# Kernel optimization log

Measured on AMD Instinct MI355X. Metric: run time of the kernel, lower is better.

The kernel has to match this reference:

```python
import jax, jax.numpy as jnp
import numpy as np

VOCAB = 65535
EMB = 1024
CTX = 1024
B = 32
HID = 4 * EMB


def setup_inputs() -> dict:
    key = jax.random.key(0)
    ks = jax.random.split(key, 20)
    s = 0.02
    inp = {
        "idx": jax.random.randint(ks[0], (B, 1), 0, VOCAB),
        "key_cache": jax.random.normal(ks[1], (B, CTX - 1, EMB), jnp.float32),
        "value_cache": jax.random.normal(ks[2], (B, CTX - 1, EMB), jnp.float32),
        "emb_table": jax.random.normal(ks[3], (VOCAB, EMB), jnp.float32) * s,
        "pos_table": jax.random.normal(ks[4], (CTX, EMB), jnp.float32) * s,
        "Wk": jax.random.normal(ks[5], (EMB, EMB), jnp.float32) * s,
        "bk": jnp.zeros((EMB,), jnp.float32),
        "Wv": jax.random.normal(ks[6], (EMB, EMB), jnp.float32) * s,
        "bv": jnp.zeros((EMB,), jnp.float32),
        "Wq": jax.random.normal(ks[7], (EMB, EMB), jnp.float32) * s,
        "bq": jnp.zeros((EMB,), jnp.float32),
        "W1": jax.random.normal(ks[8], (EMB, HID), jnp.float32) * s,
        "b1": jnp.zeros((HID,), jnp.float32),
        "W2": jax.random.normal(ks[9], (HID, EMB), jnp.float32) * s,
        "b2": jnp.zeros((EMB,), jnp.float32),
        "Wl": jax.random.normal(ks[10], (EMB, VOCAB), jnp.float32) * s,
        "bl": jnp.zeros((VOCAB,), jnp.float32),
    }
    return inp


def reference(idx, key_cache, value_cache, emb_table, pos_table,
              Wk, bk, Wv, bv, Wq, bq, W1, b1, W2, b2, Wl, bl):
    # token + position embeddings (seq_len=1, positions = arange(1) = [0])
    tok = emb_table[idx]                      # [B, 1, D]
    pos = pos_table[:1][None, :, :]           # [1, 1, D]
    x = tok + pos                             # [B, 1, D]

    # cache truncation to last context_size-1 steps (no-op here at 1023)
    kc = key_cache[:, -(CTX - 1):, :]
    vc = value_cache[:, -(CTX - 1):, :]

    # single-head attention with KV cache
    k_new = x @ Wk + bk                       # [B, 1, D]
    v_new = x @ Wv + bv
    q_new = x @ Wq + bq
    keys = jnp.concatenate([kc, k_new], axis=1)    # [B, S, D]
    values = jnp.concatenate([vc, v_new], axis=1)  # [B, S, D]
    scale = 1.0 / jnp.sqrt(jnp.asarray(EMB, x.dtype))
    scores = jnp.einsum("bqd,bsd->bqs", q_new, keys) * scale  # [B, 1, S]
    probs = jax.nn.softmax(scores, axis=-1)
    attn_out = jnp.einsum("bqs,bsd->bqd", probs, values)      # [B, 1, D]

    # feed-forward (exact GELU, matching torch nn.GELU default)
    h = jax.nn.gelu(attn_out @ W1 + b1, approximate=False)
    ffn_out = h @ W2 + b2                     # [B, 1, D]

    logits = ffn_out @ Wl + bl                # [B, 1, VOCAB]
    return logits
```

## Files before the change

### kernel.cpp

```cpp
#include <hip/hip_runtime.h>
#include <cstddef>

#define BATCH 32
#define EMBD 1024
#define SCTX 1023
#define CTXF 1024
#define HIDD 4096
#define VOC 65535

__global__ void embed_kernel(const int* __restrict__ idx, const float* __restrict__ emb,
                             const float* __restrict__ pos, float* __restrict__ x) {
  int b = blockIdx.x, t = threadIdx.x;
  const float4* er = (const float4*)(emb + (size_t)idx[b] * EMBD);
  const float4* pr = (const float4*)pos;
  float4 e = er[t], p = pr[t];
  ((float4*)(x + (size_t)b * EMBD))[t] = make_float4(e.x + p.x, e.y + p.y, e.z + p.z, e.w + p.w);
}

template <int CHK>
__global__ __launch_bounds__(256) void skgemm_lds(const float* __restrict__ X,
                                                  const float* __restrict__ W,
                                                  float* __restrict__ Pout, int N, int K) {
  __shared__ float xt[CHK][BATCH];
  int t = threadIdx.x;
  int p = blockIdx.y;
  int i0 = p * CHK;
  for (int m = t; m < CHK * BATCH; m += 256) {
    int i = m >> 5, b = m & 31;
    xt[i][b] = X[b * K + i0 + i];
  }
  __syncthreads();

  int j = blockIdx.x * 256 + t;
  float acc[BATCH];
#pragma unroll
  for (int b = 0; b < BATCH; ++b) acc[b] = 0.f;
  const float* wp = W + (size_t)i0 * N + j;
#pragma unroll 8
  for (int i = 0; i < CHK; ++i) {
    float w = wp[(size_t)i * N];
#pragma unroll
    for (int b = 0; b < BATCH; ++b) acc[b] = fmaf(xt[i][b], w, acc[b]);
  }
#pragma unroll
  for (int b = 0; b < BATCH; ++b) Pout[((size_t)p * BATCH + b) * N + j] = acc[b];
}

template <int CHK>
__global__ __launch_bounds__(256) void qkv_lds(const float* __restrict__ X,
                                               const float* __restrict__ Wk,
                                               const float* __restrict__ Wv,
                                               const float* __restrict__ Wq,
                                               float* __restrict__ Pout, int nch) {
  __shared__ float xt[CHK][BATCH];
  int t = threadIdx.x;
  int p = blockIdx.y;
  int i0 = p * CHK;
  for (int m = t; m < CHK * BATCH; m += 256) {
    int i = m >> 5, b = m & 31;
    xt[i][b] = X[b * EMBD + i0 + i];
  }
  __syncthreads();

  const float* __restrict__ W = (blockIdx.z == 0) ? Wk : (blockIdx.z == 1) ? Wv : Wq;
  int j = blockIdx.x * 256 + t;
  float acc[BATCH];
#pragma unroll
  for (int b = 0; b < BATCH; ++b) acc[b] = 0.f;
  const float* wp = W + (size_t)i0 * EMBD + j;
#pragma unroll 8
  for (int i = 0; i < CHK; ++i) {
    float w = wp[(size_t)i * EMBD];
#pragma unroll
    for (int b = 0; b < BATCH; ++b) acc[b] = fmaf(xt[i][b], w, acc[b]);
  }
#pragma unroll
  for (int b = 0; b < BATCH; ++b)
    Pout[((size_t)(blockIdx.z * nch + p) * BATCH + b) * EMBD + j] = acc[b];
}

__global__ void reduce_qkv(const float* __restrict__ part, int P,
                           const float* __restrict__ bk, const float* __restrict__ bv,
                           const float* __restrict__ bq,
                           float* __restrict__ kout, float* __restrict__ vout,
                           float* __restrict__ qout) {
  int z = blockIdx.y;
  int m = blockIdx.x * 256 + threadIdx.x;
  float s = 0.f;
  for (int p = 0; p < P; ++p) s += part[(size_t)(z * P + p) * (BATCH * EMBD) + m];
  const float* bias = (z == 0) ? bk : (z == 1) ? bv : bq;
  float* out = (z == 0) ? kout : (z == 1) ? vout : qout;
  out[m] = s + bias[m & (EMBD - 1)];
}

__global__ void reduce_ep(const float* __restrict__ part, int P,
                          const float* __restrict__ bias, float* __restrict__ out,
                          int total, int mask, int act) {
  int m = blockIdx.x * 256 + threadIdx.x;
  if (m >= total) return;
  float s = 0.f;
  for (int p = 0; p < P; ++p) s += part[(size_t)p * total + m];
  if (bias) s += bias[m & mask];
  if (act == 1) s = 0.5f * s * (1.f + erff(s * 0.70710678118654752f));
  out[m] = s;
}

__global__ void scores_kernel(const float* __restrict__ q, const float* __restrict__ kcache,
                              const float* __restrict__ knew, float* __restrict__ scores) {
  int b = blockIdx.y;
  int wave = threadIdx.x >> 6, lane = threadIdx.x & 63;
  const float* qb = q + (size_t)b * EMBD;
  float4 qf[4];
#pragma unroll
  for (int r = 0; r < 4; ++r) qf[r] = *(const float4*)(qb + r * 256 + lane * 4);
  int sbase = blockIdx.x * 16 + wave * 4;
  const float* kr[4];
  float acc[4] = {0.f, 0.f, 0.f, 0.f};
#pragma unroll
  for (int it = 0; it < 4; ++it) {
    int s = sbase + it;
    kr[it] = (s < SCTX) ? (kcache + ((size_t)b * SCTX + s) * EMBD)
                        : (knew + (size_t)b * EMBD);
  }
#pragma unroll
  for (int r = 0; r < 4; ++r) {
#pragma unroll
    for (int it = 0; it < 4; ++it) {
      float4 kf = *(const float4*)(kr[it] + r * 256 + lane * 4);
      acc[it] += qf[r].x * kf.x + qf[r].y * kf.y + qf[r].z * kf.z + qf[r].w * kf.w;
    }
  }
#pragma unroll
  for (int it = 0; it < 4; ++it) {
    float a = acc[it];
#pragma unroll
    for (int m = 32; m > 0; m >>= 1) a += __shfl_xor(a, m, 64);
    if (lane == 0) scores[(size_t)b * CTXF + sbase + it] = a * 0.03125f;
  }
}

__global__ void softmax_kernel(float* __restrict__ sc) {
  int b = blockIdx.x;
  int t = threadIdx.x;
  __shared__ float red[16];
  float v = sc[(size_t)b * CTXF + t];
  float m = v;
#pragma unroll
  for (int d = 32; d > 0; d >>= 1) m = fmaxf(m, __shfl_xor(m, d, 64));
  if ((t & 63) == 0) red[t >> 6] = m;
  __syncthreads();
  float bm = red[0];
#pragma unroll
  for (int w = 1; w < 16; ++w) bm = fmaxf(bm, red[w]);
  float e = expf(v - bm);
  __syncthreads();
  float s = e;
#pragma unroll
  for (int d = 32; d > 0; d >>= 1) s += __shfl_xor(s, d, 64);
  if ((t & 63) == 0) red[t >> 6] = s;
  __syncthreads();
  float bs = 0.f;
#pragma unroll
  for (int w = 0; w < 16; ++w) bs += red[w];
  sc[(size_t)b * CTXF + t] = e / bs;
}

__global__ void pv_kernel(const float* __restrict__ probs, const float* __restrict__ vcache,
                          const float* __restrict__ vnew, float* __restrict__ part) {
  int b = blockIdx.y;
  int p = blockIdx.x;
  int t = threadIdx.x;
  float acc[4] = {0.f, 0.f, 0.f, 0.f};
  int s0 = p * 32;
#pragma unroll 4
  for (int s = s0; s < s0 + 32; ++s) {
    float pr = probs[(size_t)b * CTXF + s];
    const float* vrow = (s < SCTX) ? (vcache + ((size_t)b * SCTX + s) * EMBD)
                                   : (vnew + (size_t)b * EMBD);
#pragma unroll
    for (int r = 0; r < 4; ++r) acc[r] = fmaf(pr, vrow[t + r * 256], acc[r]);
  }
#pragma unroll
  for (int r = 0; r < 4; ++r) part[((size_t)p * BATCH + b) * EMBD + t + r * 256] = acc[r];
}

__global__ __launch_bounds__(256) void logits_v3(const float* __restrict__ X,
                                                 const float* __restrict__ Wl,
                                                 float* __restrict__ part) {
  __shared__ float xt[256][BATCH];
  int t = threadIdx.x;
  int p = blockIdx.y;
  int q0 = p * 256;
  for (int m = t; m < 256 * BATCH; m += 256) {
    int i = m >> 5, b = m & 31;
    xt[i][b] = X[b * EMBD + q0 + i];
  }
  __syncthreads();

  int jb = blockIdx.x * 512;
  int j0 = jb + t;
  int j1 = jb + 256 + t;
  bool v1 = (j1 < VOC);
  float acc0[BATCH], acc1[BATCH];
#pragma unroll
  for (int b = 0; b < BATCH; ++b) { acc0[b] = 0.f; acc1[b] = 0.f; }

  const float* wp = Wl + (size_t)q0 * VOC;
#pragma unroll 4
  for (int i = 0; i < 256; ++i) {
    float w0 = wp[(size_t)i * VOC + j0];
    float w1 = v1 ? wp[(size_t)i * VOC + j1] : 0.f;
#pragma unroll
    for (int b = 0; b < BATCH; ++b) {
      float xv = xt[i][b];
      acc0[b] = fmaf(xv, w0, acc0[b]);
      acc1[b] = fmaf(xv, w1, acc1[b]);
    }
  }
#pragma unroll
  for (int b = 0; b < BATCH; ++b) {
    part[((size_t)p * BATCH + b) * VOC + j0] = acc0[b];
    if (v1) part[((size_t)p * BATCH + b) * VOC + j1] = acc1[b];
  }
}

__global__ void logits_reduce(const float* __restrict__ part, const float* __restrict__ bl,
                              float* __restrict__ out) {
  size_t m = (size_t)blockIdx.x * 256 + threadIdx.x;
  if (m >= (size_t)BATCH * VOC) return;
  int j = (int)(m % VOC);
  float s = 0.f;
#pragma unroll
  for (int p = 0; p < 4; ++p) s += part[(size_t)p * BATCH * VOC + m];
  out[m] = s + bl[j];
}

__global__ void logits_splitb(const float* __restrict__ X, const float* __restrict__ Wl,
                              const float* __restrict__ bl, float* __restrict__ out) {
  int j = blockIdx.x * 256 + threadIdx.x;
  if (j >= VOC) return;
  int b0 = blockIdx.y * 16;
  float acc[16];
#pragma unroll
  for (int b = 0; b < 16; ++b) acc[b] = 0.f;
#pragma unroll 8
  for (int i = 0; i < EMBD; ++i) {
    float w = Wl[(size_t)i * VOC + j];
#pragma unroll
    for (int b = 0; b < 16; ++b) acc[b] = fmaf(X[(b0 + b) * EMBD + i], w, acc[b]);
  }
  float bb = bl[j];
#pragma unroll
  for (int b = 0; b < 16; ++b) out[(size_t)(b0 + b) * VOC + j] = acc[b] + bb;
}

extern "C" void kernel_launch(void* const* d_in, const int* in_sizes, int n_in,
                              void* d_out, int out_size, void* d_ws, size_t ws_size,
                              hipStream_t stream) {
  const int* idx = (const int*)d_in[0];
  const float* key_cache = (const float*)d_in[1];
  const float* value_cache = (const float*)d_in[2];
  const float* emb_table = (const float*)d_in[3];
  const float* pos_table = (const float*)d_in[4];
  const float* Wk = (const float*)d_in[5];
  const float* bk = (const float*)d_in[6];
  const float* Wv = (const float*)d_in[7];
  const float* bv = (const float*)d_in[8];
  const float* Wq = (const float*)d_in[9];
  const float* bq = (const float*)d_in[10];
  const float* W1 = (const float*)d_in[11];
  const float* b1 = (const float*)d_in[12];
  const float* W2 = (const float*)d_in[13];
  const float* b2 = (const float*)d_in[14];
  const float* Wl = (const float*)d_in[15];
  const float* bl = (const float*)d_in[16];
  float* out = (float*)d_out;

  float* ws = (float*)d_ws;
  float* x    = ws;
  float* k    = ws + 32768;
  float* v    = ws + 65536;
  float* q    = ws + 98304;
  float* prob = ws + 131072;
  float* attn = ws + 163840;
  float* h    = ws + 196608;
  float* ffn  = ws + 327680;
  float* part = ws + 360448;

  size_t partCap = (ws_size / 4 > 360448) ? ws_size / 4 - 360448 : 0;

  embed_kernel<<<dim3(BATCH), 256, 0, stream>>>(idx, emb_table, pos_table, x);

  if (partCap >= (size_t)3 * 32 * BATCH * EMBD) {
    qkv_lds<32><<<dim3(4, 32, 3), 256, 0, stream>>>(x, Wk, Wv, Wq, part, 32);
    reduce_qkv<<<dim3(128, 3), 256, 0, stream>>>(part, 32, bk, bv, bq, k, v, q);
  } else {
    qkv_lds<128><<<dim3(4, 8, 3), 256, 0, stream>>>(x, Wk, Wv, Wq, part, 8);
    reduce_qkv<<<dim3(128, 3), 256, 0, stream>>>(part, 8, bk, bv, bq, k, v, q);
  }

  scores_kernel<<<dim3(64, BATCH), 256, 0, stream>>>(q, key_cache, k, prob);
  softmax_kernel<<<dim3(BATCH), 1024, 0, stream>>>(prob);
  pv_kernel<<<dim3(32, BATCH), 256, 0, stream>>>(prob, value_cache, v, part);
  reduce_ep<<<dim3(128), 256, 0, stream>>>(part, 32, nullptr, attn, BATCH * EMBD, 0, 0);

  skgemm_lds<64><<<dim3(16, 16), 256, 0, stream>>>(attn, W1, part, HIDD, EMBD);
  reduce_ep<<<dim3(512), 256, 0, stream>>>(part, 16, b1, h, BATCH * HIDD, HIDD - 1, 1);

  skgemm_lds<64><<<dim3(4, 64), 256, 0, stream>>>(h, W2, part, EMBD, HIDD);
  reduce_ep<<<dim3(128), 256, 0, stream>>>(part, 64, b2, ffn, BATCH * EMBD, EMBD - 1, 0);

  if (partCap >= (size_t)4 * BATCH * VOC) {
    logits_v3<<<dim3(128, 4), 256, 0, stream>>>(ffn, Wl, part);
    logits_reduce<<<dim3(8192), 256, 0, stream>>>(part, bl, out);
  } else {
    logits_splitb<<<dim3(256, 2), 256, 0, stream>>>(ffn, Wl, bl, out);
  }
}
```

Before: 240.6 us.

## Widen logits GEMM register tile to 4 columns and split K eight ways

The logits kernel now computes four output columns per thread (128 accumulators) instead of two, and reads x from LDS as float4. The K dimension is split into 8 chunks of 128 rather than 4 of 256, and the reduce kernel sums 8 partials. This aims to cut LDS traffic per FMA and keep the grid at 512 blocks. In exchange it raises register pressure and doubles the partial-sum write and read traffic, which is about 8 MB each way. If the partial buffer is too small, the code falls back to the slower split-batch path.

```diff
diff --git a/kernel.cpp b/kernel.cpp
--- a/kernel.cpp
+++ b/kernel.cpp
@@ -184,43 +184,65 @@
   for (int r = 0; r < 4; ++r) part[((size_t)p * BATCH + b) * EMBD + t + r * 256] = acc[r];
 }
 
-__global__ __launch_bounds__(256) void logits_v3(const float* __restrict__ X,
-                                                 const float* __restrict__ Wl,
-                                                 float* __restrict__ part) {
-  __shared__ float xt[256][BATCH];
+__global__ __launch_bounds__(256, 2) void logits_v4(const float* __restrict__ X,
+                                                    const float* __restrict__ Wl,
+                                                    float* __restrict__ part) {
+  __shared__ float xt[128][BATCH];
   int t = threadIdx.x;
   int p = blockIdx.y;
-  int q0 = p * 256;
-  for (int m = t; m < 256 * BATCH; m += 256) {
+  int q0 = p * 128;
+  for (int m = t; m < 128 * BATCH; m += 256) {
     int i = m >> 5, b = m & 31;
     xt[i][b] = X[b * EMBD + q0 + i];
   }
   __syncthreads();
 
-  int jb = blockIdx.x * 512;
+  int jb = blockIdx.x * 1024;
   int j0 = jb + t;
   int j1 = jb + 256 + t;
-  bool v1 = (j1 < VOC);
-  float acc0[BATCH], acc1[BATCH];
-#pragma unroll
-  for (int b = 0; b < BATCH; ++b) { acc0[b] = 0.f; acc1[b] = 0.f; }
+  int j2 = jb + 512 + t;
+  int j3 = jb + 768 + t;
+  bool v3 = (j3 < VOC);
+  float acc0[BATCH], acc1[BATCH], acc2[BATCH], acc3[BATCH];
+#pragma unroll
+  for (int b = 0; b < BATCH; ++b) { acc0[b] = 0.f; acc1[b] = 0.f; acc2[b] = 0.f; acc3[b] = 0.f; }
 
   const float* wp = Wl + (size_t)q0 * VOC;
 #pragma unroll 4
-  for (int i = 0; i < 256; ++i) {
-    float w0 = wp[(size_t)i * VOC + j0];
-    float w1 = v1 ? wp[(size_t)i * VOC + j1] : 0.f;
-#pragma unroll
-    for (int b = 0; b < BATCH; ++b) {
-      float xv = xt[i][b];
-      acc0[b] = fmaf(xv, w0, acc0[b]);
-      acc1[b] = fmaf(xv, w1, acc1[b]);
+  for (int i = 0; i < 128; ++i) {
+    const float* wr = wp + (size_t)i * VOC;
+    float w0 = wr[j0];
+    float w1 = wr[j1];
+    float w2 = wr[j2];
+    float w3 = v3 ? wr[j3] : 0.f;
+#pragma unroll
+    for (int b4 = 0; b4 < 8; ++b4) {
+      float4 xv = *(const float4*)&xt[i][b4 * 4];
+      acc0[b4 * 4 + 0] = fmaf(xv.x, w0, acc0[b4 * 4 + 0]);
+      acc0[b4 * 4 + 1] = fmaf(xv.y, w0, acc0[b4 * 4 + 1]);
+      acc0[b4 * 4 + 2] = fmaf(xv.z, w0, acc0[b4 * 4 + 2]);
+      acc0[b4 * 4 + 3] = fmaf(xv.w, w0, acc0[b4 * 4 + 3]);
+      acc1[b4 * 4 + 0] = fmaf(xv.x, w1, acc1[b4 * 4 + 0]);
+      acc1[b4 * 4 + 1] = fmaf(xv.y, w1, acc1[b4 * 4 + 1]);
+      acc1[b4 * 4 + 2] = fmaf(xv.z, w1, acc1[b4 * 4 + 2]);
+      acc1[b4 * 4 + 3] = fmaf(xv.w, w1, acc1[b4 * 4 + 3]);
+      acc2[b4 * 4 + 0] = fmaf(xv.x, w2, acc2[b4 * 4 + 0]);
+      acc2[b4 * 4 + 1] = fmaf(xv.y, w2, acc2[b4 * 4 + 1]);
+      acc2[b4 * 4 + 2] = fmaf(xv.z, w2, acc2[b4 * 4 + 2]);
+      acc2[b4 * 4 + 3] = fmaf(xv.w, w2, acc2[b4 * 4 + 3]);
+      acc3[b4 * 4 + 0] = fmaf(xv.x, w3, acc3[b4 * 4 + 0]);
+      acc3[b4 * 4 + 1] = fmaf(xv.y, w3, acc3[b4 * 4 + 1]);
+      acc3[b4 * 4 + 2] = fmaf(xv.z, w3, acc3[b4 * 4 + 2]);
+      acc3[b4 * 4 + 3] = fmaf(xv.w, w3, acc3[b4 * 4 + 3]);
     }
   }
 #pragma unroll
   for (int b = 0; b < BATCH; ++b) {
-    part[((size_t)p * BATCH + b) * VOC + j0] = acc0[b];
-    if (v1) part[((size_t)p * BATCH + b) * VOC + j1] = acc1[b];
+    float* pr = part + ((size_t)p * BATCH + b) * VOC;
+    pr[j0] = acc0[b];
+    pr[j1] = acc1[b];
+    pr[j2] = acc2[b];
+    if (v3) pr[j3] = acc3[b];
   }
 }
 
@@ -231,7 +253,7 @@
   int j = (int)(m % VOC);
   float s = 0.f;
 #pragma unroll
-  for (int p = 0; p < 4; ++p) s += part[(size_t)p * BATCH * VOC + m];
+  for (int p = 0; p < 8; ++p) s += part[(size_t)p * BATCH * VOC + m];
   out[m] = s + bl[j];
 }
 
@@ -310,8 +332,8 @@
   skgemm_lds<64><<<dim3(4, 64), 256, 0, stream>>>(h, W2, part, EMBD, HIDD);
   reduce_ep<<<dim3(128), 256, 0, stream>>>(part, 64, b2, ffn, BATCH * EMBD, EMBD - 1, 0);
 
-  if (partCap >= (size_t)4 * BATCH * VOC) {
-    logits_v3<<<dim3(128, 4), 256, 0, stream>>>(ffn, Wl, part);
+  if (partCap >= (size_t)8 * BATCH * VOC) {
+    logits_v4<<<dim3(64, 8), 256, 0, stream>>>(ffn, Wl, part);
     logits_reduce<<<dim3(8192), 256, 0, stream>>>(part, bl, out);
   } else {
     logits_splitb<<<dim3(256, 2), 256, 0, stream>>>(ffn, Wl, bl, out);
```

New measurement: 258.2 us. 1.07x slower.
